# Performance work log

Hardware: AMD Instinct MI355X
Metric: run time of the kernel (lower is better)

Reference implementation:

```python
import jax, jax.numpy as jnp
import numpy as np

B, IN, H = 8192, 1024, 2048

def setup_inputs() -> dict:
    key = jax.random.key(0)
    ks = jax.random.split(key, 9)
    s_g = 1.0 / np.sqrt(IN + H)
    s_r = 1.0 / np.sqrt(IN)
    return {
        "x_t": jax.random.normal(ks[0], (B, IN), jnp.float32),
        "h_t_1": jax.random.normal(ks[1], (B, H), jnp.float32),
        "c_t_1": jax.random.normal(ks[2], (B, H), jnp.float32),
        # stacked gate weights [4, IN+H, H] in order (input, forget, output, c_hat)
        "W_gates": jax.random.uniform(ks[3], (4, IN + H, H), jnp.float32, -s_g, s_g),
        "b_gates": jax.random.uniform(ks[4], (4, H), jnp.float32, -s_g, s_g),
        "W_res": jax.random.uniform(ks[5], (IN, H), jnp.float32, -s_r, s_r),
        "b_res": jax.random.uniform(ks[6], (H,), jnp.float32, -s_r, s_r),
    }

def reference(x_t, h_t_1, c_t_1, W_gates, b_gates, W_res, b_res):
    xh = jnp.concatenate([x_t, h_t_1], axis=1)            # [B, IN+H]
    # one batched GEMM for all 4 gates: [B, IN+H] x [4, IN+H, H] -> [4, B, H]
    gates = jnp.einsum('bk,gkh->gbh', xh, W_gates) + b_gates[:, None, :]
    i_t = jax.nn.sigmoid(gates[0])
    f_t = jax.nn.sigmoid(gates[1])
    o_t = jax.nn.sigmoid(gates[2])
    c_hat = jnp.tanh(gates[3])
    c_t = f_t * c_t_1 + i_t * c_hat
    x_res = x_t @ W_res + b_res                            # input_size != hidden_size
    h_t = o_t * jnp.tanh(c_t) + x_res
    return h_t, c_t
```

## Files before the change

### kernel.cpp

```cpp
#include <hip/hip_runtime.h>
#include <cstdint>
#include <cstddef>

#define Bsz 8192
#define INsz 1024
#define Hsz 2048
#define Kxh 3072

typedef __attribute__((ext_vector_type(8))) short bf16x8;
typedef __attribute__((ext_vector_type(4))) float f32x4;

__device__ __forceinline__ unsigned short f2bf(float f) {
  unsigned int u = __float_as_uint(f);
  u += 0x7FFFu + ((u >> 16) & 1u);
  return (unsigned short)(u >> 16);
}

__device__ __forceinline__ void gload_lds16(const void* g, void* l) {
  __builtin_amdgcn_global_load_lds(
      (const __attribute__((address_space(1))) void*)g,
      (__attribute__((address_space(3))) void*)l, 16, 0, 0);
}

__device__ __forceinline__ float fsigmoid(float x) { return 1.f / (1.f + __expf(-x)); }
__device__ __forceinline__ float ftanh(float x) {
  float ax = fabsf(x);
  float t = __expf(-2.f * ax);
  float r = (1.f - t) / (1.f + t);
  return copysignf(r, x);
}

__global__ void convert_xh_kernel(const float* __restrict__ x,
                                  const float* __restrict__ h,
                                  unsigned short* __restrict__ xh) {
  int chunk = blockIdx.x * 256 + threadIdx.x;
  int row = chunk / 384;
  int c8 = (chunk - row * 384) * 8;
  const float* src = (c8 < INsz) ? (x + (size_t)row * INsz + c8)
                                 : (h + (size_t)row * Hsz + (c8 - INsz));
  f32x4 v0 = *(const f32x4*)src;
  f32x4 v1 = *(const f32x4*)(src + 4);
  bf16x8 o;
  o[0] = (short)f2bf(v0[0]); o[1] = (short)f2bf(v0[1]);
  o[2] = (short)f2bf(v0[2]); o[3] = (short)f2bf(v0[3]);
  o[4] = (short)f2bf(v1[0]); o[5] = (short)f2bf(v1[1]);
  o[6] = (short)f2bf(v1[2]); o[7] = (short)f2bf(v1[3]);
  *(bf16x8*)(xh + (size_t)chunk * 8) = o;
}

__global__ void transpose_conv_kernel(const float* __restrict__ W,
                                      unsigned short* __restrict__ WT,
                                      int K, int N) {
  __shared__ float tile[64][65];
  const size_t moff = (size_t)blockIdx.z * (size_t)K * N;
  int n0 = blockIdx.x * 64;
  int k0 = blockIdx.y * 64;
  int t = threadIdx.x;
  #pragma unroll
  for (int j = 0; j < 4; ++j) {
    int idx = j * 256 + t;
    int row = idx >> 4;
    int c4 = (idx & 15) * 4;
    f32x4 v = *(const f32x4*)&W[moff + (size_t)(k0 + row) * N + n0 + c4];
    tile[row][c4 + 0] = v[0];
    tile[row][c4 + 1] = v[1];
    tile[row][c4 + 2] = v[2];
    tile[row][c4 + 3] = v[3];
  }
  __syncthreads();
  #pragma unroll
  for (int j = 0; j < 2; ++j) {
    int idx = j * 256 + t;
    int nr = idx >> 3;
    int kc = (idx & 7) * 8;
    bf16x8 o;
    #pragma unroll
    for (int i = 0; i < 8; ++i) o[i] = (short)f2bf(tile[kc + i][nr]);
    *(bf16x8*)&WT[moff + (size_t)(n0 + nr) * K + k0 + kc] = o;
  }
}

__device__ __forceinline__ void gemm_pass(
    const unsigned short* __restrict__ A,
    const unsigned short* __restrict__ Bt,
    int ldb, int K,
    short* lA, short* lB,
    int tid, int lane, int wr, int wc,
    f32x4 (&acc)[4][4])
{
  const int il = lane & 15;
  const int kl = (lane >> 4) * 8;
  const int axor = (il & 7) << 3;
  for (int k0 = 0; k0 < K; k0 += 64) {
    #pragma unroll
    for (int c = 0; c < 4; ++c) {
      int ch = c * 256 + tid;
      int row = ch >> 3;
      int scc = (ch & 7) ^ (row & 7);
      gload_lds16(A + (size_t)row * Kxh + k0 + scc * 8, lA + ch * 8);
    }
    #pragma unroll
    for (int c = 0; c < 4; ++c) {
      int ch = c * 256 + tid;
      int row = ch >> 3;
      int scc = (ch & 7) ^ (row & 7);
      gload_lds16(Bt + (size_t)row * ldb + k0 + scc * 8, lB + ch * 8);
    }
    __syncthreads();
    #pragma unroll
    for (int ks = 0; ks < 2; ++ks) {
      bf16x8 a[4], b[4];
      #pragma unroll
      for (int m = 0; m < 4; ++m)
        a[m] = *(const bf16x8*)&lA[(wr * 64 + m * 16 + il) * 64 + ((ks * 32 + kl) ^ axor)];
      #pragma unroll
      for (int n = 0; n < 4; ++n)
        b[n] = *(const bf16x8*)&lB[(wc * 64 + n * 16 + il) * 64 + ((ks * 32 + kl) ^ axor)];
      #pragma unroll
      for (int m = 0; m < 4; ++m)
        #pragma unroll
        for (int n = 0; n < 4; ++n)
          acc[m][n] = __builtin_amdgcn_mfma_f32_16x16x32_bf16(a[m], b[n], acc[m][n], 0, 0, 0);
    }
    __syncthreads();
  }
}

__global__ __launch_bounds__(256, 2) void lstm_fused_kernel(
    const unsigned short* __restrict__ xh,
    const unsigned short* __restrict__ WgT,
    const unsigned short* __restrict__ WrT,
    const float* __restrict__ c_prev,
    const float* __restrict__ b_gates,
    const float* __restrict__ b_res,
    float* __restrict__ h_out,
    float* __restrict__ c_out)
{
  __shared__ alignas(16) short lA[128 * 64];
  __shared__ alignas(16) short lB[128 * 64];
  const int tid = threadIdx.x;
  const int lane = tid & 63;
  const int wid = tid >> 6;
  const int wr = wid >> 1, wc = wid & 1;

  const int orig = blockIdx.x;
  const int wg = (orig & 7) * 128 + (orig >> 3);
  const int bcol = (wg >> 6) * 128;
  const int brow = (wg & 63) * 128;

  const unsigned short* Ab = xh + (size_t)brow * Kxh;
  const int col0 = bcol + wc * 64 + (lane & 15);
  const int row0 = brow + wr * 64 + ((lane >> 4) << 2);

  const f32x4 zf = {0.f, 0.f, 0.f, 0.f};
  f32x4 acc[4][4];
  f32x4 C[4][4];
  f32x4 I[4][4];

  #pragma unroll
  for (int m = 0; m < 4; ++m)
    #pragma unroll
    for (int n = 0; n < 4; ++n) acc[m][n] = zf;
  gemm_pass(Ab, WgT + (size_t)(1 * Hsz + bcol) * Kxh, Kxh, Kxh, lA, lB, tid, lane, wr, wc, acc);
  #pragma unroll
  for (int n = 0; n < 4; ++n) {
    float bgn = b_gates[1 * Hsz + col0 + n * 16];
    #pragma unroll
    for (int m = 0; m < 4; ++m)
      #pragma unroll
      for (int r = 0; r < 4; ++r) {
        float f = fsigmoid(acc[m][n][r] + bgn);
        C[m][n][r] = f * c_prev[(size_t)(row0 + m * 16 + r) * Hsz + col0 + n * 16];
      }
  }

  #pragma unroll
  for (int m = 0; m < 4; ++m)
    #pragma unroll
    for (int n = 0; n < 4; ++n) acc[m][n] = zf;
  gemm_pass(Ab, WgT + (size_t)(0 * Hsz + bcol) * Kxh, Kxh, Kxh, lA, lB, tid, lane, wr, wc, acc);
  #pragma unroll
  for (int n = 0; n < 4; ++n) {
    float bgn = b_gates[0 * Hsz + col0 + n * 16];
    #pragma unroll
    for (int m = 0; m < 4; ++m)
      #pragma unroll
      for (int r = 0; r < 4; ++r)
        I[m][n][r] = fsigmoid(acc[m][n][r] + bgn);
  }

  #pragma unroll
  for (int m = 0; m < 4; ++m)
    #pragma unroll
    for (int n = 0; n < 4; ++n) acc[m][n] = zf;
  gemm_pass(Ab, WgT + (size_t)(3 * Hsz + bcol) * Kxh, Kxh, Kxh, lA, lB, tid, lane, wr, wc, acc);
  #pragma unroll
  for (int n = 0; n < 4; ++n) {
    float bgn = b_gates[3 * Hsz + col0 + n * 16];
    #pragma unroll
    for (int m = 0; m < 4; ++m)
      #pragma unroll
      for (int r = 0; r < 4; ++r) {
        float ct = C[m][n][r] + I[m][n][r] * ftanh(acc[m][n][r] + bgn);
        c_out[(size_t)(row0 + m * 16 + r) * Hsz + col0 + n * 16] = ct;
        C[m][n][r] = ftanh(ct);
      }
  }

  #pragma unroll
  for (int m = 0; m < 4; ++m)
    #pragma unroll
    for (int n = 0; n < 4; ++n) acc[m][n] = zf;
  gemm_pass(Ab, WgT + (size_t)(2 * Hsz + bcol) * Kxh, Kxh, Kxh, lA, lB, tid, lane, wr, wc, acc);
  #pragma unroll
  for (int n = 0; n < 4; ++n) {
    float bgn = b_gates[2 * Hsz + col0 + n * 16];
    #pragma unroll
    for (int m = 0; m < 4; ++m)
      #pragma unroll
      for (int r = 0; r < 4; ++r)
        C[m][n][r] = fsigmoid(acc[m][n][r] + bgn) * C[m][n][r];
  }

  #pragma unroll
  for (int m = 0; m < 4; ++m)
    #pragma unroll
    for (int n = 0; n < 4; ++n) acc[m][n] = zf;
  gemm_pass(Ab, WrT + (size_t)bcol * INsz, INsz, INsz, lA, lB, tid, lane, wr, wc, acc);
  #pragma unroll
  for (int n = 0; n < 4; ++n) {
    float brn = b_res[col0 + n * 16];
    #pragma unroll
    for (int m = 0; m < 4; ++m)
      #pragma unroll
      for (int r = 0; r < 4; ++r)
        h_out[(size_t)(row0 + m * 16 + r) * Hsz + col0 + n * 16] =
            C[m][n][r] + acc[m][n][r] + brn;
  }
}

extern "C" void kernel_launch(void* const* d_in, const int* in_sizes, int n_in,
                              void* d_out, int out_size, void* d_ws, size_t ws_size,
                              hipStream_t stream) {
  const float* x  = (const float*)d_in[0];
  const float* h  = (const float*)d_in[1];
  const float* c  = (const float*)d_in[2];
  const float* Wg = (const float*)d_in[3];
  const float* bg = (const float*)d_in[4];
  const float* Wr = (const float*)d_in[5];
  const float* br = (const float*)d_in[6];
  float* out = (float*)d_out;

  char* ws = (char*)d_ws;
  unsigned short* xh  = (unsigned short*)ws;
  unsigned short* WgT = (unsigned short*)(ws + 50331648);
  unsigned short* WrT = (unsigned short*)(ws + 100663296);

  convert_xh_kernel<<<12288, 256, 0, stream>>>(x, h, xh);
  transpose_conv_kernel<<<dim3(32, 48, 4), 256, 0, stream>>>(Wg, WgT, Kxh, Hsz);
  transpose_conv_kernel<<<dim3(32, 16, 1), 256, 0, stream>>>(Wr, WrT, INsz, Hsz);

  lstm_fused_kernel<<<1024, 256, 0, stream>>>(
      xh, WgT, WrT, c, bg, br, out, out + (size_t)Bsz * Hsz);
}
```

Baseline: 1.011 ms.

## Split fused LSTM into pipelined 256x256 GEMM plus separate elementwise epilogue

Replaces the single fused kernel, which ran five sequential unpipelined GEMM passes per 128x128 tile, with one large-tile GEMM kernel. It uses 512 threads, 256x256 tiles, double-buffered LDS, async global-to-LDS prefetch overlapped with MFMA, and setprio scheduling. All four gate planes plus the residual are treated as one wide N dimension. Gate pre-activations are stored as bf16 and the residual as fp32 into the output, then a separate elementwise kernel applies biases and nonlinearities. This raises data reuse and compute/load overlap, at the cost of extra HBM traffic for the intermediate gates and an added bf16 rounding of the pre-activations.

Result: faster. 911.6 us (-9.8%).

```diff
diff --git a/kernel.cpp b/kernel.cpp
--- a/kernel.cpp
+++ b/kernel.cpp
@@ -14,6 +14,9 @@
   unsigned int u = __float_as_uint(f);
   u += 0x7FFFu + ((u >> 16) & 1u);
   return (unsigned short)(u >> 16);
+}
+__device__ __forceinline__ float bf2f(short s) {
+  return __uint_as_float((unsigned int)(unsigned short)s << 16);
 }
 
 __device__ __forceinline__ void gload_lds16(const void* g, void* l) {
@@ -80,163 +83,214 @@
   }
 }
 
-__device__ __forceinline__ void gemm_pass(
-    const unsigned short* __restrict__ A,
-    const unsigned short* __restrict__ Bt,
-    int ldb, int K,
-    short* lA, short* lB,
-    int tid, int lane, int wr, int wc,
-    f32x4 (&acc)[4][4])
-{
-  const int il = lane & 15;
-  const int kl = (lane >> 4) * 8;
-  const int axor = (il & 7) << 3;
-  for (int k0 = 0; k0 < K; k0 += 64) {
-    #pragma unroll
-    for (int c = 0; c < 4; ++c) {
-      int ch = c * 256 + tid;
-      int row = ch >> 3;
-      int scc = (ch & 7) ^ (row & 7);
-      gload_lds16(A + (size_t)row * Kxh + k0 + scc * 8, lA + ch * 8);
-    }
-    #pragma unroll
-    for (int c = 0; c < 4; ++c) {
-      int ch = c * 256 + tid;
-      int row = ch >> 3;
-      int scc = (ch & 7) ^ (row & 7);
-      gload_lds16(Bt + (size_t)row * ldb + k0 + scc * 8, lB + ch * 8);
-    }
-    __syncthreads();
-    #pragma unroll
-    for (int ks = 0; ks < 2; ++ks) {
-      bf16x8 a[4], b[4];
-      #pragma unroll
-      for (int m = 0; m < 4; ++m)
-        a[m] = *(const bf16x8*)&lA[(wr * 64 + m * 16 + il) * 64 + ((ks * 32 + kl) ^ axor)];
-      #pragma unroll
-      for (int n = 0; n < 4; ++n)
-        b[n] = *(const bf16x8*)&lB[(wc * 64 + n * 16 + il) * 64 + ((ks * 32 + kl) ^ axor)];
-      #pragma unroll
-      for (int m = 0; m < 4; ++m)
-        #pragma unroll
-        for (int n = 0; n < 4; ++n)
-          acc[m][n] = __builtin_amdgcn_mfma_f32_16x16x32_bf16(a[m], b[n], acc[m][n], 0, 0, 0);
-    }
-    __syncthreads();
-  }
-}
-
-__global__ __launch_bounds__(256, 2) void lstm_fused_kernel(
+__device__ __forceinline__ int lds_chunk(int row, int c) {
+  return (row << 2) | (c ^ ((row & 3) ^ ((row >> 2) & 3)));
+}
+
+__global__ __launch_bounds__(512, 2) void gemm_gates_kernel(
     const unsigned short* __restrict__ xh,
     const unsigned short* __restrict__ WgT,
     const unsigned short* __restrict__ WrT,
+    unsigned short* __restrict__ gates,
+    float* __restrict__ res_out)
+{
+  __shared__ short lA[2][2][8192];
+  __shared__ short lB[2][2][8192];
+  const int tid = threadIdx.x;
+  const int lane = tid & 63;
+  const int wid = tid >> 6;
+  const int wm = wid >> 2, wn = wid & 3;
+  const int il = lane & 15, kl = lane >> 4;
+
+  const int orig = blockIdx.x;
+  const int xcd = orig & 7;
+  const int idx = orig >> 3;
+  const int bcol_t = ((idx >> 5) << 3) + xcd;
+  const int brow_t = idx & 31;
+  const int brow = brow_t * 256;
+  const int bcol = bcol_t * 256;
+  const int plane = bcol >> 11;
+  const int pcol = bcol & 2047;
+
+  const unsigned short* Ag = xh + (size_t)brow * Kxh;
+  const unsigned short* Bg;
+  int ldb, K;
+  if (plane < 4) { Bg = WgT + ((size_t)plane * Hsz + pcol) * Kxh; ldb = Kxh; K = Kxh; }
+  else           { Bg = WrT + (size_t)pcol * INsz;                ldb = INsz; K = INsz; }
+  const int nt = K >> 6;
+
+  const int r0 = tid >> 2;
+  const int r1 = r0 + 128;
+  const int c0 = (tid & 3) ^ ((r0 & 3) ^ ((r0 >> 2) & 3));
+  const int c1 = (tid & 3) ^ ((r1 & 3) ^ ((r1 >> 2) & 3));
+  const size_t a_off0 = (size_t)r0 * Kxh + c0 * 8;
+  const size_t a_off1 = (size_t)r1 * Kxh + c1 * 8;
+  const size_t b_off0 = (size_t)r0 * (size_t)ldb + c0 * 8;
+  const size_t b_off1 = (size_t)r1 * (size_t)ldb + c1 * 8;
+  const int lds_t0 = tid * 8;
+  const int lds_t1 = (tid + 512) * 8;
+
+  const int a_row = wm * 128 + il;
+  const int b_row = wn * 64 + il;
+
+  f32x4 acc[8][4];
+  #pragma unroll
+  for (int m = 0; m < 8; ++m)
+    #pragma unroll
+    for (int n = 0; n < 4; ++n) acc[m][n] = f32x4{0.f, 0.f, 0.f, 0.f};
+
+  gload_lds16(Ag + a_off0,      &lA[0][0][lds_t0]);
+  gload_lds16(Ag + a_off1,      &lA[0][0][lds_t1]);
+  gload_lds16(Bg + b_off0,      &lB[0][0][lds_t0]);
+  gload_lds16(Bg + b_off1,      &lB[0][0][lds_t1]);
+  gload_lds16(Ag + a_off0 + 32, &lA[0][1][lds_t0]);
+  gload_lds16(Ag + a_off1 + 32, &lA[0][1][lds_t1]);
+  gload_lds16(Bg + b_off0 + 32, &lB[0][1][lds_t0]);
+  gload_lds16(Bg + b_off1 + 32, &lB[0][1][lds_t1]);
+
+  for (int t = 0; t < nt; ++t) {
+    const int cur = t & 1, nxt = cur ^ 1;
+    const bool pf = (t + 1) < nt;
+    const int kpre = (t + 1) << 6;
+    bf16x8 bq[4], af[4];
+
+    __builtin_amdgcn_sched_barrier(0);
+    asm volatile("s_waitcnt vmcnt(4)" ::: "memory");
+    asm volatile("s_barrier" ::: "memory");
+    __builtin_amdgcn_sched_barrier(0);
+    #pragma unroll
+    for (int n = 0; n < 4; ++n)
+      bq[n] = *(const bf16x8*)&lB[cur][0][lds_chunk(b_row + n * 16, kl) * 8];
+    #pragma unroll
+    for (int m = 0; m < 4; ++m)
+      af[m] = *(const bf16x8*)&lA[cur][0][lds_chunk(a_row + m * 16, kl) * 8];
+    if (pf) {
+      gload_lds16(Ag + a_off0 + kpre, &lA[nxt][0][lds_t0]);
+      gload_lds16(Ag + a_off1 + kpre, &lA[nxt][0][lds_t1]);
+    }
+    __builtin_amdgcn_s_setprio(1);
+    #pragma unroll
+    for (int m = 0; m < 4; ++m)
+      #pragma unroll
+      for (int n = 0; n < 4; ++n)
+        acc[m][n] = __builtin_amdgcn_mfma_f32_16x16x32_bf16(af[m], bq[n], acc[m][n], 0, 0, 0);
+    __builtin_amdgcn_s_setprio(0);
+
+    #pragma unroll
+    for (int m = 0; m < 4; ++m)
+      af[m] = *(const bf16x8*)&lA[cur][0][lds_chunk(a_row + (m + 4) * 16, kl) * 8];
+    if (pf) {
+      gload_lds16(Bg + b_off0 + kpre, &lB[nxt][0][lds_t0]);
+      gload_lds16(Bg + b_off1 + kpre, &lB[nxt][0][lds_t1]);
+    }
+    __builtin_amdgcn_s_setprio(1);
+    #pragma unroll
+    for (int m = 0; m < 4; ++m)
+      #pragma unroll
+      for (int n = 0; n < 4; ++n)
+        acc[m + 4][n] = __builtin_amdgcn_mfma_f32_16x16x32_bf16(af[m], bq[n], acc[m + 4][n], 0, 0, 0);
+    __builtin_amdgcn_s_setprio(0);
+
+    __builtin_amdgcn_sched_barrier(0);
+    asm volatile("s_waitcnt vmcnt(4)" ::: "memory");
+    asm volatile("s_barrier" ::: "memory");
+    __builtin_amdgcn_sched_barrier(0);
+    #pragma unroll
+    for (int n = 0; n < 4; ++n)
+      bq[n] = *(const bf16x8*)&lB[cur][1][lds_chunk(b_row + n * 16, kl) * 8];
+    #pragma unroll
+    for (int m = 0; m < 4; ++m)
+      af[m] = *(const bf16x8*)&lA[cur][1][lds_chunk(a_row + m * 16, kl) * 8];
+    if (pf) {
+      gload_lds16(Ag + a_off0 + kpre + 32, &lA[nxt][1][lds_t0]);
+      gload_lds16(Ag + a_off1 + kpre + 32, &lA[nxt][1][lds_t1]);
+    }
+    __builtin_amdgcn_s_setprio(1);
+    #pragma unroll
+    for (int m = 0; m < 4; ++m)
+      #pragma unroll
+      for (int n = 0; n < 4; ++n)
+        acc[m][n] = __builtin_amdgcn_mfma_f32_16x16x32_bf16(af[m], bq[n], acc[m][n], 0, 0, 0);
+    __builtin_amdgcn_s_setprio(0);
+
+    #pragma unroll
+    for (int m = 0; m < 4; ++m)
+      af[m] = *(const bf16x8*)&lA[cur][1][lds_chunk(a_row + (m + 4) * 16, kl) * 8];
+    if (pf) {
+      gload_lds16(Bg + b_off0 + kpre + 32, &lB[nxt][1][lds_t0]);
+      gload_lds16(Bg + b_off1 + kpre + 32, &lB[nxt][1][lds_t1]);
+    }
+    __builtin_amdgcn_s_setprio(1);
+    #pragma unroll
+    for (int m = 0; m < 4; ++m)
+      #pragma unroll
+      for (int n = 0; n < 4; ++n)
+        acc[m + 4][n] = __builtin_amdgcn_mfma_f32_16x16x32_bf16(af[m], bq[n], acc[m + 4][n], 0, 0, 0);
+    __builtin_amdgcn_s_setprio(0);
+  }
+
+  const int g_row0 = brow + wm * 128 + kl * 4;
+  if (plane < 4) {
+    unsigned short* gp = gates + (size_t)plane * ((size_t)Bsz * Hsz);
+    #pragma unroll
+    for (int m = 0; m < 8; ++m)
+      #pragma unroll
+      for (int n = 0; n < 4; ++n) {
+        int col = pcol + wn * 64 + n * 16 + il;
+        #pragma unroll
+        for (int r = 0; r < 4; ++r)
+          gp[(size_t)(g_row0 + m * 16 + r) * Hsz + col] = f2bf(acc[m][n][r]);
+      }
+  } else {
+    #pragma unroll
+    for (int m = 0; m < 8; ++m)
+      #pragma unroll
+      for (int n = 0; n < 4; ++n) {
+        int col = pcol + wn * 64 + n * 16 + il;
+        #pragma unroll
+        for (int r = 0; r < 4; ++r)
+          res_out[(size_t)(g_row0 + m * 16 + r) * Hsz + col] = acc[m][n][r];
+      }
+  }
+}
+
+__global__ __launch_bounds__(256) void lstm_epilogue_kernel(
+    const unsigned short* __restrict__ gates,
     const float* __restrict__ c_prev,
     const float* __restrict__ b_gates,
     const float* __restrict__ b_res,
     float* __restrict__ h_out,
     float* __restrict__ c_out)
 {
-  __shared__ alignas(16) short lA[128 * 64];
-  __shared__ alignas(16) short lB[128 * 64];
-  const int tid = threadIdx.x;
-  const int lane = tid & 63;
-  const int wid = tid >> 6;
-  const int wr = wid >> 1, wc = wid & 1;
-
-  const int orig = blockIdx.x;
-  const int wg = (orig & 7) * 128 + (orig >> 3);
-  const int bcol = (wg >> 6) * 128;
-  const int brow = (wg & 63) * 128;
-
-  const unsigned short* Ab = xh + (size_t)brow * Kxh;
-  const int col0 = bcol + wc * 64 + (lane & 15);
-  const int row0 = brow + wr * 64 + ((lane >> 4) << 2);
-
-  const f32x4 zf = {0.f, 0.f, 0.f, 0.f};
-  f32x4 acc[4][4];
-  f32x4 C[4][4];
-  f32x4 I[4][4];
-
+  const size_t plane = (size_t)Bsz * Hsz;
+  int idx = blockIdx.x * 256 + threadIdx.x;
+  size_t base = (size_t)idx * 8;
+  int hcol = (idx & 255) * 8;
+  bf16x8 gi = *(const bf16x8*)(gates + 0 * plane + base);
+  bf16x8 gf = *(const bf16x8*)(gates + 1 * plane + base);
+  bf16x8 go = *(const bf16x8*)(gates + 2 * plane + base);
+  bf16x8 gc = *(const bf16x8*)(gates + 3 * plane + base);
+  f32x4 cp0 = *(const f32x4*)(c_prev + base);
+  f32x4 cp1 = *(const f32x4*)(c_prev + base + 4);
+  f32x4 rs0 = *(const f32x4*)(h_out + base);
+  f32x4 rs1 = *(const f32x4*)(h_out + base + 4);
+  f32x4 h0, h1, c0, c1;
   #pragma unroll
-  for (int m = 0; m < 4; ++m)
-    #pragma unroll
-    for (int n = 0; n < 4; ++n) acc[m][n] = zf;
-  gemm_pass(Ab, WgT + (size_t)(1 * Hsz + bcol) * Kxh, Kxh, Kxh, lA, lB, tid, lane, wr, wc, acc);
-  #pragma unroll
-  for (int n = 0; n < 4; ++n) {
-    float bgn = b_gates[1 * Hsz + col0 + n * 16];
-    #pragma unroll
-    for (int m = 0; m < 4; ++m)
-      #pragma unroll
-      for (int r = 0; r < 4; ++r) {
-        float f = fsigmoid(acc[m][n][r] + bgn);
-        C[m][n][r] = f * c_prev[(size_t)(row0 + m * 16 + r) * Hsz + col0 + n * 16];
-      }
-  }
-
-  #pragma unroll
-  for (int m = 0; m < 4; ++m)
-    #pragma unroll
-    for (int n = 0; n < 4; ++n) acc[m][n] = zf;
-  gemm_pass(Ab, WgT + (size_t)(0 * Hsz + bcol) * Kxh, Kxh, Kxh, lA, lB, tid, lane, wr, wc, acc);
-  #pragma unroll
-  for (int n = 0; n < 4; ++n) {
-    float bgn = b_gates[0 * Hsz + col0 + n * 16];
-    #pragma unroll
-    for (int m = 0; m < 4; ++m)
-      #pragma unroll
-      for (int r = 0; r < 4; ++r)
-        I[m][n][r] = fsigmoid(acc[m][n][r] + bgn);
-  }
-
-  #pragma unroll
-  for (int m = 0; m < 4; ++m)
-    #pragma unroll
-    for (int n = 0; n < 4; ++n) acc[m][n] = zf;
-  gemm_pass(Ab, WgT + (size_t)(3 * Hsz + bcol) * Kxh, Kxh, Kxh, lA, lB, tid, lane, wr, wc, acc);
-  #pragma unroll
-  for (int n = 0; n < 4; ++n) {
-    float bgn = b_gates[3 * Hsz + col0 + n * 16];
-    #pragma unroll
-    for (int m = 0; m < 4; ++m)
-      #pragma unroll
-      for (int r = 0; r < 4; ++r) {
-        float ct = C[m][n][r] + I[m][n][r] * ftanh(acc[m][n][r] + bgn);
-        c_out[(size_t)(row0 + m * 16 + r) * Hsz + col0 + n * 16] = ct;
-        C[m][n][r] = ftanh(ct);
-      }
-  }
-
-  #pragma unroll
-  for (int m = 0; m < 4; ++m)
-    #pragma unroll
-    for (int n = 0; n < 4; ++n) acc[m][n] = zf;
-  gemm_pass(Ab, WgT + (size_t)(2 * Hsz + bcol) * Kxh, Kxh, Kxh, lA, lB, tid, lane, wr, wc, acc);
-  #pragma unroll
-  for (int n = 0; n < 4; ++n) {
-    float bgn = b_gates[2 * Hsz + col0 + n * 16];
-    #pragma unroll
-    for (int m = 0; m < 4; ++m)
-      #pragma unroll
-      for (int r = 0; r < 4; ++r)
-        C[m][n][r] = fsigmoid(acc[m][n][r] + bgn) * C[m][n][r];
-  }
-
-  #pragma unroll
-  for (int m = 0; m < 4; ++m)
-    #pragma unroll
-    for (int n = 0; n < 4; ++n) acc[m][n] = zf;
-  gemm_pass(Ab, WrT + (size_t)bcol * INsz, INsz, INsz, lA, lB, tid, lane, wr, wc, acc);
-  #pragma unroll
-  for (int n = 0; n < 4; ++n) {
-    float brn = b_res[col0 + n * 16];
-    #pragma unroll
-    for (int m = 0; m < 4; ++m)
-      #pragma unroll
-      for (int r = 0; r < 4; ++r)
-        h_out[(size_t)(row0 + m * 16 + r) * Hsz + col0 + n * 16] =
-            C[m][n][r] + acc[m][n][r] + brn;
-  }
+  for (int j = 0; j < 8; ++j) {
+    float ig = fsigmoid(bf2f(gi[j]) + b_gates[0 * Hsz + hcol + j]);
+    float fg = fsigmoid(bf2f(gf[j]) + b_gates[1 * Hsz + hcol + j]);
+    float og = fsigmoid(bf2f(go[j]) + b_gates[2 * Hsz + hcol + j]);
+    float ch = ftanh  (bf2f(gc[j]) + b_gates[3 * Hsz + hcol + j]);
+    float cp = (j < 4) ? cp0[j] : cp1[j - 4];
+    float rs = ((j < 4) ? rs0[j] : rs1[j - 4]) + b_res[hcol + j];
+    float ct = fg * cp + ig * ch;
+    float ht = og * ftanh(ct) + rs;
+    if (j < 4) { c0[j] = ct; h0[j] = ht; } else { c1[j - 4] = ct; h1[j - 4] = ht; }
+  }
+  *(f32x4*)(h_out + base)     = h0;
+  *(f32x4*)(h_out + base + 4) = h1;
+  *(f32x4*)(c_out + base)     = c0;
+  *(f32x4*)(c_out + base + 4) = c1;
 }
 
 extern "C" void kernel_launch(void* const* d_in, const int* in_sizes, int n_in,
@@ -252,14 +306,17 @@
   float* out = (float*)d_out;
 
   char* ws = (char*)d_ws;
-  unsigned short* xh  = (unsigned short*)ws;
-  unsigned short* WgT = (unsigned short*)(ws + 50331648);
-  unsigned short* WrT = (unsigned short*)(ws + 100663296);
+  unsigned short* xh    = (unsigned short*)ws;
+  unsigned short* WgT   = (unsigned short*)(ws + 50331648);
+  unsigned short* WrT   = (unsigned short*)(ws + 100663296);
+  unsigned short* gates = (unsigned short*)(ws + 104857600);
 
   convert_xh_kernel<<<12288, 256, 0, stream>>>(x, h, xh);
   transpose_conv_kernel<<<dim3(32, 48, 4), 256, 0, stream>>>(Wg, WgT, Kxh, Hsz);
   transpose_conv_kernel<<<dim3(32, 16, 1), 256, 0, stream>>>(Wr, WrT, INsz, Hsz);
 
-  lstm_fused_kernel<<<1024, 256, 0, stream>>>(
-      xh, WgT, WrT, c, bg, br, out, out + (size_t)Bsz * Hsz);
-}
+  gemm_gates_kernel<<<1280, 512, 0, stream>>>(xh, WgT, WrT, gates, out);
+
+  lstm_epilogue_kernel<<<8192, 256, 0, stream>>>(
+      gates, c, bg, br, out, out + (size_t)Bsz * Hsz);
+}
```
